# Performance work log

Measured on AMD Instinct MI355X. Metric: run time of the kernel, lower is better.

## Reference

```python
import jax, jax.numpy as jnp
import numpy as np
from jax import lax

B, L, V, E, H = 256, 512, 256, 256, 1024


def setup_inputs() -> dict:
    key = jax.random.key(0)
    k1, k2, k3, k4, k5 = jax.random.split(key, 5)
    x = jax.random.randint(k1, (B, L), 0, V, dtype=jnp.int64)
    hidden = jnp.zeros((B, H), dtype=jnp.float32)
    emb_table = jax.random.normal(k2, (V, E), dtype=jnp.float32)  # nn.Embedding default init ~N(0,1)
    W_e = 0.01 * jax.random.normal(k3, (E, H), dtype=jnp.float32)
    W_h = 0.01 * jax.random.normal(k4, (H, H), dtype=jnp.float32)
    W_o = 0.01 * jax.random.normal(k5, (H, V), dtype=jnp.float32)
    return {"x": x, "hidden": hidden, "emb_table": emb_table, "W_e": W_e, "W_h": W_h, "W_o": W_o}


def reference(x, hidden, emb_table, W_e, W_h, W_o):
    # Precompute input projection for all timesteps in one batched GEMM:
    # emb_table[x] : [B, L, E];  x_proj : [L, B, H] (time-major for scan)
    x_proj = jnp.einsum('ble,eh->lbh', emb_table[x], W_e)

    def step(h_prev, x_t):
        h_t = jnp.tanh(x_t + h_prev @ W_h)  # [B, H]
        return h_t, h_t

    final_hidden, outs = lax.scan(step, hidden, x_proj)  # outs: [L, B, H]
    # logits: [B, L, V]
    logits = jnp.einsum('lbh,hv->blv', outs, W_o)
    return logits, final_hidden
```

## Files before the change

### kernel.cpp

```cpp
#include <hip/hip_runtime.h>
#include <hip/hip_bf16.h>
#include <math.h>

#define B_ 256
#define L_ 512
#define V_ 256
#define E_ 256
#define H_ 1024
#define NSTEP_ 513

typedef float  f32x4  __attribute__((ext_vector_type(4)));
typedef short  bf16x8 __attribute__((ext_vector_type(8)));

static __device__ __forceinline__ ushort f2bf(float v) {
    __hip_bfloat16 b = __float2bfloat16(v);
    return *reinterpret_cast<ushort*>(&b);
}

__global__ void k_transpose_bf16(const float* __restrict__ in, ushort* __restrict__ out,
                                 int R, int C) {
    __shared__ float tile[64][65];
    int bx = blockIdx.x;
    int by = blockIdx.y;
    int tid = threadIdx.x;
    int g = tid >> 6, l = tid & 63;
    for (int i = 0; i < 16; ++i) {
        int r = g * 16 + i;
        tile[r][l] = in[(size_t)(by * 64 + r) * C + bx * 64 + l];
    }
    __syncthreads();
    for (int i = 0; i < 16; ++i) {
        int c = g * 16 + i;
        out[(size_t)(bx * 64 + c) * R + by * 64 + l] = f2bf(tile[l][c]);
    }
}

__global__ void k_f32_to_bf16(const float* __restrict__ in, ushort* __restrict__ out, int n) {
    int i = blockIdx.x * blockDim.x + threadIdx.x;
    if (i < n) out[i] = f2bf(in[i]);
}

__global__ void k_zero(unsigned* __restrict__ p, int n) {
    int i = blockIdx.x * blockDim.x + threadIdx.x;
    if (i < n) p[i] = 0u;
}

__global__ void k_proj(const float* __restrict__ emb, const float* __restrict__ We,
                       float* __restrict__ proj) {
    __shared__ float er[E_];
    int t = blockIdx.x;
    int h = blockIdx.y * 256 + threadIdx.x;
    er[threadIdx.x] = emb[t * E_ + threadIdx.x];
    __syncthreads();
    float acc = 0.f;
#pragma unroll 8
    for (int e = 0; e < E_; ++e) acc += er[e] * We[(size_t)e * H_ + h];
    proj[(size_t)t * H_ + h] = acc;
}

__global__ __launch_bounds__(256, 1) void k_scan(
    const int* __restrict__ x, const float* __restrict__ proj,
    const ushort* __restrict__ WhT, const ushort* __restrict__ WoT,
    ushort* __restrict__ ring, float* __restrict__ logits,
    float* __restrict__ final_h, unsigned* __restrict__ flags)
{
    __shared__ ushort lds_w[32 * 1024];
    __shared__ ushort lds_h[32 * 1024];
    __shared__ float  red[256 * 5];
    __shared__ ushort stile[32 * 32];

    int tid = threadIdx.x;
    int w = tid >> 6, lane = tid & 63;
    int l15 = lane & 15, l4 = lane >> 4;
    int bid = blockIdx.x;
    int rg = bid & 7;
    int cg = bid >> 3;
    int r0 = rg * 32, c0 = cg * 32;

    {
        const char* wsrc = (const char*)(WhT + (size_t)c0 * H_);
        char* wd = (char*)lds_w;
        for (int i = 0; i < 16; ++i) {
            int chunk = (w * 16 + i) * 1024;
            int o = chunk + lane * 16;
            int row = o >> 11, b = o & 2047;
            int so = row * 2048 + (b ^ ((row & 7) << 4));
            __builtin_amdgcn_global_load_lds(
                (const __attribute__((address_space(1))) void*)(wsrc + so),
                (__attribute__((address_space(3))) void*)(wd + chunk), 16, 0, 0);
        }
    }

    int a = w >> 1, bc = w & 1;
    int arow = a * 16 + l15;
    int brow = bc * 16 + l15;
    const char* ha = (const char*)lds_h + arow * 2048;
    const char* wa = (const char*)lds_w + brow * 2048;
    int as = (arow & 7) << 4, bs = (brow & 7) << 4;
    int gcol = c0 + bc * 16 + l15;

    int lrg = cg & 1, vcol0 = (cg >> 1) * 16;
    int srow = lrg * 16 + l15;
    const char* hbp = (const char*)lds_h + srow * 2048;
    int hs2 = (srow & 7) << 4;
    const ushort* wo = WoT + (size_t)(vcol0 + l15) * H_;
    int bbase = (w == 1) ? 0 : (w == 2) ? 11 : 22;
    int bcnt  = (w == 3) ? 10 : 11;

    for (int s = 0; s <= NSTEP_; ++s) {
        float pv[4];
        if (s < L_) {
#pragma unroll
            for (int j = 0; j < 4; ++j) {
                int grow = r0 + a * 16 + l4 * 4 + j;
                pv[j] = proj[(size_t)x[grow * L_ + s] * H_ + gcol];
            }
        }

        if (w == 0) {
            if (s >= 1 && s <= L_) {
                const unsigned* fp = flags + ((size_t)rg * NSTEP_ + s) * 32 + lane;
                unsigned v = 1u;
                while (true) {
                    if (lane < 32) {
                        asm volatile("global_load_dword %0, %1, off sc0 sc1\n\t"
                                     "s_waitcnt vmcnt(0)"
                                     : "=v"(v) : "v"(fp) : "memory");
                    }
                    if (__ballot(v != 0u) == ~0ull) break;
                }
            }
        } else if (s >= 2) {
            f32x4 lacc = {0.f, 0.f, 0.f, 0.f};
            for (int kk = 0; kk < bcnt; ++kk) {
                int k = (bbase + kk) * 32 + l4 * 8;
                bf16x8 af = *(const bf16x8*)(hbp + ((2 * k) ^ hs2));
                bf16x8 bf = *(const bf16x8*)(wo + k);
                lacc = __builtin_amdgcn_mfma_f32_16x16x32_bf16(af, bf, lacc, 0, 0, 0);
            }
#pragma unroll
            for (int j = 0; j < 4; ++j) red[tid * 5 + j] = lacc[j];
        }
        __syncthreads();

        f32x4 tv[16];
        if (s <= L_) {
            const char* hsrc = (const char*)(ring + (size_t)(s & 1) * B_ * H_
                                             + (size_t)r0 * H_) + tid * 16;
#pragma unroll
            for (int i = 0; i < 16; ++i) {
                asm volatile("global_load_dwordx4 %0, %1, off sc0 sc1"
                             : "=v"(tv[i]) : "v"(hsrc + i * 4096) : "memory");
            }
        }
        if (w == 0 && s >= 2) {
            int growb = r0 + lrg * 16 + l4 * 4;
#pragma unroll
            for (int j = 0; j < 4; ++j) {
                float ssum = red[(64 + lane) * 5 + j] + red[(128 + lane) * 5 + j]
                           + red[(192 + lane) * 5 + j];
                logits[((size_t)(growb + j) * L_ + (s - 2)) * V_ + vcol0 + l15] = ssum;
            }
        }
        if (s <= L_) {
            asm volatile("s_waitcnt vmcnt(0)" ::: "memory");
#pragma unroll
            for (int i = 0; i < 16; ++i) {
                int o = i * 4096 + tid * 16;
                int row = o >> 11, b = o & 2047;
                *(f32x4*)((char*)lds_h + row * 2048 + (b ^ ((row & 7) << 4))) = tv[i];
            }
        }
        __syncthreads();

        if (s < L_) {
            f32x4 acc0 = {0.f, 0.f, 0.f, 0.f};
            f32x4 acc1 = {0.f, 0.f, 0.f, 0.f};
#pragma unroll
            for (int kk = 0; kk < 32; kk += 2) {
                int kb0 = (kk * 32 + l4 * 8) * 2;
                int kb1 = ((kk + 1) * 32 + l4 * 8) * 2;
                bf16x8 af0 = *(const bf16x8*)(ha + (kb0 ^ as));
                bf16x8 bf0 = *(const bf16x8*)(wa + (kb0 ^ bs));
                bf16x8 af1 = *(const bf16x8*)(ha + (kb1 ^ as));
                bf16x8 bf1 = *(const bf16x8*)(wa + (kb1 ^ bs));
                acc0 = __builtin_amdgcn_mfma_f32_16x16x32_bf16(af0, bf0, acc0, 0, 0, 0);
                acc1 = __builtin_amdgcn_mfma_f32_16x16x32_bf16(af1, bf1, acc1, 0, 0, 0);
            }
#pragma unroll
            for (int j = 0; j < 4; ++j) {
                int lrow = a * 16 + l4 * 4 + j;
                float hv = tanhf((acc0[j] + acc1[j]) + pv[j]);
                stile[lrow * 32 + bc * 16 + l15] = f2bf(hv);
                if (s == L_ - 1) final_h[(size_t)(r0 + lrow) * H_ + gcol] = hv;
            }
            __syncthreads();
            if (tid < 128) {
                int row = tid >> 2, seg = tid & 3;
                f32x4 d = *(const f32x4*)&stile[row * 32 + seg * 8];
                char* dst = (char*)(ring + (size_t)((s + 1) & 1) * B_ * H_
                                    + (size_t)(r0 + row) * H_ + c0 + seg * 8);
                asm volatile("global_store_dwordx4 %0, %1, off sc0 sc1"
                             :: "v"(dst), "v"(d) : "memory");
            }
            asm volatile("s_waitcnt vmcnt(0)" ::: "memory");
            __syncthreads();
            if (tid == 0) {
                unsigned* fdst = flags + ((size_t)rg * NSTEP_ + (s + 1)) * 32 + cg;
                unsigned one = 1u;
                asm volatile("global_store_dword %0, %1, off sc0 sc1"
                             :: "v"(fdst), "v"(one) : "memory");
            }
        }
    }
}

extern "C" void kernel_launch(void* const* d_in, const int* in_sizes, int n_in,
                              void* d_out, int out_size, void* d_ws, size_t ws_size,
                              hipStream_t stream)
{
    const int*   x   = (const int*)d_in[0];
    const float* hid = (const float*)d_in[1];
    const float* emb = (const float*)d_in[2];
    const float* We  = (const float*)d_in[3];
    const float* Wh  = (const float*)d_in[4];
    const float* Wo  = (const float*)d_in[5];

    float* logits  = (float*)d_out;
    float* final_h = logits + (size_t)B_ * L_ * V_;

    char* ws = (char*)d_ws;
    float*    proj  = (float*)(ws);
    ushort*   WhT   = (ushort*)(ws + (1u << 20));
    ushort*   WoT   = (ushort*)(ws + 3u * (1u << 20));
    ushort*   ring  = (ushort*)(ws + 3u * (1u << 20) + (1u << 19));
    unsigned* flags = (unsigned*)(ws + 4u * (1u << 20) + (1u << 19));

    k_zero<<<dim3(NSTEP_), 256, 0, stream>>>(flags, 8 * NSTEP_ * 32);
    k_transpose_bf16<<<dim3(16, 16), 256, 0, stream>>>(Wh, WhT, H_, H_);
    k_transpose_bf16<<<dim3(4, 16),  256, 0, stream>>>(Wo, WoT, H_, V_);
    k_f32_to_bf16<<<dim3(1024), 256, 0, stream>>>(hid, ring, B_ * H_);
    k_proj<<<dim3(256, 4), 256, 0, stream>>>(emb, We, proj);

    k_scan<<<dim3(256), 256, 0, stream>>>(x, proj, WhT, WoT, ring,
                                          logits, final_h, flags);
}
```

Baseline: 2.433 ms.

## Split logits projection out of recurrent scan into chunked GEMM kernels over hidden-state ring

Before, each scan step also computed a slice of the output projection inside the persistent recurrence kernel. Now the scan kernel only runs the recurrence over chunks of timesteps and writes every hidden state into a multi-slot ring buffer. A separate k_logits kernel then computes the logits for each chunk as a larger batched GEMM. It also replaces tanhf with an exp-based tanh, shrinks the flags to bytes, and pads the staging tile. This shortens the serial critical path per step, but adds per-chunk kernel relaunches, reloads of the weight panel, and dependence on workspace size for the ring.

```diff
diff --git a/kernel.cpp b/kernel.cpp
--- a/kernel.cpp
+++ b/kernel.cpp
@@ -7,21 +7,26 @@
 #define V_ 256
 #define E_ 256
 #define H_ 1024
-#define NSTEP_ 513
 
 typedef float  f32x4  __attribute__((ext_vector_type(4)));
 typedef short  bf16x8 __attribute__((ext_vector_type(8)));
+typedef unsigned int u32;
+typedef unsigned char u8;
 
 static __device__ __forceinline__ ushort f2bf(float v) {
     __hip_bfloat16 b = __float2bfloat16(v);
     return *reinterpret_cast<ushort*>(&b);
 }
 
+static __device__ __forceinline__ float ftanh(float z) {
+    float e = __expf(2.f * z);
+    return 1.f - 2.f / (e + 1.f);
+}
+
 __global__ void k_transpose_bf16(const float* __restrict__ in, ushort* __restrict__ out,
                                  int R, int C) {
     __shared__ float tile[64][65];
-    int bx = blockIdx.x;
-    int by = blockIdx.y;
+    int bx = blockIdx.x, by = blockIdx.y;
     int tid = threadIdx.x;
     int g = tid >> 6, l = tid & 63;
     for (int i = 0; i < 16; ++i) {
@@ -40,7 +45,7 @@
     if (i < n) out[i] = f2bf(in[i]);
 }
 
-__global__ void k_zero(unsigned* __restrict__ p, int n) {
+__global__ void k_zero(u32* __restrict__ p, int n) {
     int i = blockIdx.x * blockDim.x + threadIdx.x;
     if (i < n) p[i] = 0u;
 }
@@ -59,22 +64,20 @@
 }
 
 __global__ __launch_bounds__(256, 1) void k_scan(
-    const int* __restrict__ x, const float* __restrict__ proj,
-    const ushort* __restrict__ WhT, const ushort* __restrict__ WoT,
-    ushort* __restrict__ ring, float* __restrict__ logits,
-    float* __restrict__ final_h, unsigned* __restrict__ flags)
+    const int* __restrict__ xs, const float* __restrict__ proj,
+    const ushort* __restrict__ WhT, ushort* __restrict__ ring,
+    float* __restrict__ final_h, u8* __restrict__ flags,
+    int t0, int Tc, int S)
 {
     __shared__ ushort lds_w[32 * 1024];
-    __shared__ ushort lds_h[32 * 1024];
-    __shared__ float  red[256 * 5];
-    __shared__ ushort stile[32 * 32];
+    __shared__ ushort panel[32 * 1024];
+    __shared__ ushort stile[32 * 40];
 
     int tid = threadIdx.x;
     int w = tid >> 6, lane = tid & 63;
     int l15 = lane & 15, l4 = lane >> 4;
     int bid = blockIdx.x;
-    int rg = bid & 7;
-    int cg = bid >> 3;
+    int rg = bid & 7, cg = bid >> 3;
     int r0 = rg * 32, c0 = cg * 32;
 
     {
@@ -92,127 +95,148 @@
     }
 
     int a = w >> 1, bc = w & 1;
-    int arow = a * 16 + l15;
-    int brow = bc * 16 + l15;
-    const char* ha = (const char*)lds_h + arow * 2048;
+    int arow = a * 16 + l15, brow = bc * 16 + l15;
+    const char* ha = (const char*)panel + arow * 2048;
     const char* wa = (const char*)lds_w + brow * 2048;
-    int as = (arow & 7) << 4, bs = (brow & 7) << 4;
+    int as_ = (arow & 7) << 4, bs = (brow & 7) << 4;
     int gcol = c0 + bc * 16 + l15;
 
-    int lrg = cg & 1, vcol0 = (cg >> 1) * 16;
-    int srow = lrg * 16 + l15;
-    const char* hbp = (const char*)lds_h + srow * 2048;
-    int hs2 = (srow & 7) << 4;
-    const ushort* wo = WoT + (size_t)(vcol0 + l15) * H_;
-    int bbase = (w == 1) ? 0 : (w == 2) ? 11 : 22;
-    int bcnt  = (w == 3) ? 10 : 11;
-
-    for (int s = 0; s <= NSTEP_; ++s) {
-        float pv[4];
-        if (s < L_) {
-#pragma unroll
-            for (int j = 0; j < 4; ++j) {
-                int grow = r0 + a * 16 + l4 * 4 + j;
-                pv[j] = proj[(size_t)x[grow * L_ + s] * H_ + gcol];
+    for (int s = 0; s < Tc; ++s) {
+        int t = t0 + s;
+        if (s > 0 && w == 0) {
+            const u8* fp = flags + (size_t)t * 256 + rg * 32 + lane;
+            u32 v = 1u;
+            while (true) {
+                if (lane < 32)
+                    asm volatile("global_load_ubyte %0, %1, off sc0 sc1\n\t"
+                                 "s_waitcnt vmcnt(0)" : "=v"(v) : "v"(fp) : "memory");
+                if (__ballot(v != 0u) == ~0ull) break;
             }
         }
-
-        if (w == 0) {
-            if (s >= 1 && s <= L_) {
-                const unsigned* fp = flags + ((size_t)rg * NSTEP_ + s) * 32 + lane;
-                unsigned v = 1u;
-                while (true) {
-                    if (lane < 32) {
-                        asm volatile("global_load_dword %0, %1, off sc0 sc1\n\t"
-                                     "s_waitcnt vmcnt(0)"
-                                     : "=v"(v) : "v"(fp) : "memory");
-                    }
-                    if (__ballot(v != 0u) == ~0ull) break;
-                }
-            }
-        } else if (s >= 2) {
-            f32x4 lacc = {0.f, 0.f, 0.f, 0.f};
-            for (int kk = 0; kk < bcnt; ++kk) {
-                int k = (bbase + kk) * 32 + l4 * 8;
-                bf16x8 af = *(const bf16x8*)(hbp + ((2 * k) ^ hs2));
-                bf16x8 bf = *(const bf16x8*)(wo + k);
-                lacc = __builtin_amdgcn_mfma_f32_16x16x32_bf16(af, bf, lacc, 0, 0, 0);
-            }
-#pragma unroll
-            for (int j = 0; j < 4; ++j) red[tid * 5 + j] = lacc[j];
-        }
-        __syncthreads();
-
-        f32x4 tv[16];
-        if (s <= L_) {
-            const char* hsrc = (const char*)(ring + (size_t)(s & 1) * B_ * H_
+        __syncthreads();
+
+        {
+            const char* hsrc = (const char*)(ring + (size_t)(t % S) * B_ * H_
                                              + (size_t)r0 * H_) + tid * 16;
-#pragma unroll
-            for (int i = 0; i < 16; ++i) {
-                asm volatile("global_load_dwordx4 %0, %1, off sc0 sc1"
+            f32x4 tv[16];
+#pragma unroll
+            for (int i = 0; i < 16; ++i)
+                asm volatile("global_load_dwordx4 %0, %1, off sc0"
                              : "=v"(tv[i]) : "v"(hsrc + i * 4096) : "memory");
-            }
-        }
-        if (w == 0 && s >= 2) {
-            int growb = r0 + lrg * 16 + l4 * 4;
-#pragma unroll
-            for (int j = 0; j < 4; ++j) {
-                float ssum = red[(64 + lane) * 5 + j] + red[(128 + lane) * 5 + j]
-                           + red[(192 + lane) * 5 + j];
-                logits[((size_t)(growb + j) * L_ + (s - 2)) * V_ + vcol0 + l15] = ssum;
-            }
-        }
-        if (s <= L_) {
             asm volatile("s_waitcnt vmcnt(0)" ::: "memory");
+            __builtin_amdgcn_sched_barrier(0);
 #pragma unroll
             for (int i = 0; i < 16; ++i) {
                 int o = i * 4096 + tid * 16;
                 int row = o >> 11, b = o & 2047;
-                *(f32x4*)((char*)lds_h + row * 2048 + (b ^ ((row & 7) << 4))) = tv[i];
+                *(f32x4*)((char*)panel + row * 2048 + (b ^ ((row & 7) << 4))) = tv[i];
             }
         }
         __syncthreads();
 
-        if (s < L_) {
-            f32x4 acc0 = {0.f, 0.f, 0.f, 0.f};
-            f32x4 acc1 = {0.f, 0.f, 0.f, 0.f};
-#pragma unroll
-            for (int kk = 0; kk < 32; kk += 2) {
-                int kb0 = (kk * 32 + l4 * 8) * 2;
-                int kb1 = ((kk + 1) * 32 + l4 * 8) * 2;
-                bf16x8 af0 = *(const bf16x8*)(ha + (kb0 ^ as));
-                bf16x8 bf0 = *(const bf16x8*)(wa + (kb0 ^ bs));
-                bf16x8 af1 = *(const bf16x8*)(ha + (kb1 ^ as));
-                bf16x8 bf1 = *(const bf16x8*)(wa + (kb1 ^ bs));
-                acc0 = __builtin_amdgcn_mfma_f32_16x16x32_bf16(af0, bf0, acc0, 0, 0, 0);
-                acc1 = __builtin_amdgcn_mfma_f32_16x16x32_bf16(af1, bf1, acc1, 0, 0, 0);
-            }
-#pragma unroll
-            for (int j = 0; j < 4; ++j) {
-                int lrow = a * 16 + l4 * 4 + j;
-                float hv = tanhf((acc0[j] + acc1[j]) + pv[j]);
-                stile[lrow * 32 + bc * 16 + l15] = f2bf(hv);
-                if (s == L_ - 1) final_h[(size_t)(r0 + lrow) * H_ + gcol] = hv;
-            }
-            __syncthreads();
-            if (tid < 128) {
-                int row = tid >> 2, seg = tid & 3;
-                f32x4 d = *(const f32x4*)&stile[row * 32 + seg * 8];
-                char* dst = (char*)(ring + (size_t)((s + 1) & 1) * B_ * H_
-                                    + (size_t)(r0 + row) * H_ + c0 + seg * 8);
-                asm volatile("global_store_dwordx4 %0, %1, off sc0 sc1"
-                             :: "v"(dst), "v"(d) : "memory");
-            }
-            asm volatile("s_waitcnt vmcnt(0)" ::: "memory");
-            __syncthreads();
-            if (tid == 0) {
-                unsigned* fdst = flags + ((size_t)rg * NSTEP_ + (s + 1)) * 32 + cg;
-                unsigned one = 1u;
-                asm volatile("global_store_dword %0, %1, off sc0 sc1"
-                             :: "v"(fdst), "v"(one) : "memory");
-            }
-        }
-    }
+        float pv[4];
+#pragma unroll
+        for (int j = 0; j < 4; ++j) {
+            int grow = r0 + a * 16 + l4 * 4 + j;
+            pv[j] = proj[(size_t)xs[grow * L_ + t] * H_ + gcol];
+        }
+        f32x4 acc0 = {0.f,0.f,0.f,0.f}, acc1 = {0.f,0.f,0.f,0.f};
+#pragma unroll
+        for (int kk = 0; kk < 32; kk += 2) {
+            int kb0 = (kk * 32 + l4 * 8) * 2;
+            int kb1 = ((kk + 1) * 32 + l4 * 8) * 2;
+            bf16x8 af0 = *(const bf16x8*)(ha + (kb0 ^ as_));
+            bf16x8 bf0 = *(const bf16x8*)(wa + (kb0 ^ bs));
+            bf16x8 af1 = *(const bf16x8*)(ha + (kb1 ^ as_));
+            bf16x8 bf1 = *(const bf16x8*)(wa + (kb1 ^ bs));
+            acc0 = __builtin_amdgcn_mfma_f32_16x16x32_bf16(af0, bf0, acc0, 0, 0, 0);
+            acc1 = __builtin_amdgcn_mfma_f32_16x16x32_bf16(af1, bf1, acc1, 0, 0, 0);
+        }
+#pragma unroll
+        for (int j = 0; j < 4; ++j) {
+            int lrow = a * 16 + l4 * 4 + j;
+            float hv = ftanh((acc0[j] + acc1[j]) + pv[j]);
+            stile[lrow * 40 + bc * 16 + l15] = f2bf(hv);
+            if (t == L_ - 1) final_h[(size_t)(r0 + lrow) * H_ + gcol] = hv;
+        }
+        __syncthreads();
+
+        if (tid < 128) {
+            int row = tid >> 2, seg = tid & 3;
+            f32x4 d = *(const f32x4*)&stile[row * 40 + seg * 8];
+            char* dst = (char*)(ring + (size_t)((t + 1) % S) * B_ * H_
+                                + (size_t)(r0 + row) * H_ + c0 + seg * 8);
+            asm volatile("global_store_dwordx4 %0, %1, off sc0 sc1"
+                         :: "v"(dst), "v"(d) : "memory");
+        }
+        asm volatile("s_waitcnt vmcnt(0)" ::: "memory");
+        __syncthreads();
+        if (tid == 0) {
+            u8* fdst = flags + (size_t)(t + 1) * 256 + rg * 32 + cg;
+            u32 one = 1u;
+            asm volatile("global_store_byte %0, %1, off sc0 sc1"
+                         :: "v"(fdst), "v"(one) : "memory");
+        }
+    }
+}
+
+__global__ __launch_bounds__(256, 1) void k_logits(
+    const ushort* __restrict__ ring, const ushort* __restrict__ WoT,
+    float* __restrict__ logits, int t0, int S)
+{
+    __shared__ ushort Ap[64 * 1024];
+    int tid = threadIdx.x;
+    int w = tid >> 6, lane = tid & 63;
+    int l15 = lane & 15, l4 = lane >> 4;
+    int bid = blockIdx.x;
+    int tl = bid >> 2, q = bid & 3;
+    int t = t0 + tl, slot = (t + 1) % S;
+
+    {
+        const char* asrc = (const char*)(ring + (size_t)slot * B_ * H_
+                                         + (size_t)(q * 64) * H_);
+        char* ad = (char*)Ap;
+        for (int i = 0; i < 32; ++i) {
+            int chunk = (w * 32 + i) * 1024;
+            int o = chunk + lane * 16;
+            int row = o >> 11, b = o & 2047;
+            int so = row * 2048 + (b ^ ((row & 7) << 4));
+            __builtin_amdgcn_global_load_lds(
+                (const __attribute__((address_space(1))) void*)(asrc + so),
+                (__attribute__((address_space(3))) void*)(ad + chunk), 16, 0, 0);
+        }
+    }
+    asm volatile("s_waitcnt vmcnt(0)" ::: "memory");
+    __syncthreads();
+
+    int arow = w * 16 + l15;
+    const char* ha = (const char*)Ap + (size_t)arow * 2048;
+    int as_ = (arow & 7) << 4;
+    bf16x8 af[32];
+#pragma unroll
+    for (int kk = 0; kk < 32; ++kk) {
+        int kb = (kk * 32 + l4 * 8) * 2;
+        af[kk] = *(const bf16x8*)(ha + (kb ^ as_));
+    }
+    f32x4 acc[16];
+#pragma unroll
+    for (int vs = 0; vs < 16; ++vs) acc[vs] = (f32x4){0.f, 0.f, 0.f, 0.f};
+    const ushort* wob = WoT + (size_t)l15 * H_ + l4 * 8;
+#pragma unroll
+    for (int kk = 0; kk < 32; ++kk) {
+#pragma unroll
+        for (int vs = 0; vs < 16; ++vs) {
+            bf16x8 bfr = *(const bf16x8*)(wob + (size_t)(vs * 16) * H_ + kk * 32);
+            acc[vs] = __builtin_amdgcn_mfma_f32_16x16x32_bf16(af[kk], bfr, acc[vs], 0, 0, 0);
+        }
+    }
+#pragma unroll
+    for (int vs = 0; vs < 16; ++vs)
+#pragma unroll
+        for (int j = 0; j < 4; ++j) {
+            int brow = q * 64 + w * 16 + l4 * 4 + j;
+            logits[(size_t)brow * (L_ * V_) + (size_t)t * V_ + vs * 16 + l15] = acc[vs][j];
+        }
 }
 
 extern "C" void kernel_launch(void* const* d_in, const int* in_sizes, int n_in,
@@ -230,18 +254,29 @@
     float* final_h = logits + (size_t)B_ * L_ * V_;
 
     char* ws = (char*)d_ws;
-    float*    proj  = (float*)(ws);
-    ushort*   WhT   = (ushort*)(ws + (1u << 20));
-    ushort*   WoT   = (ushort*)(ws + 3u * (1u << 20));
-    ushort*   ring  = (ushort*)(ws + 3u * (1u << 20) + (1u << 19));
-    unsigned* flags = (unsigned*)(ws + 4u * (1u << 20) + (1u << 19));
-
-    k_zero<<<dim3(NSTEP_), 256, 0, stream>>>(flags, 8 * NSTEP_ * 32);
+    float*  proj  = (float*)(ws);
+    ushort* WhT   = (ushort*)(ws + (1u << 20));
+    ushort* WoT   = (ushort*)(ws + 3u * (1u << 20));
+    u8*     flags = (u8*)(ws + 3u * (1u << 20) + (1u << 19));
+    const size_t RING_OFF = 3u * (1u << 20) + (1u << 19) + (1u << 18);
+    ushort* ring  = (ushort*)(ws + RING_OFF);
+    const size_t SLOT = (size_t)B_ * H_ * 2u;
+
+    int S = (int)(ws_size > RING_OFF ? (ws_size - RING_OFF) / SLOT : 0);
+    if (S > 65) S = 65;
+    if (S < 2)  S = 2;
+
+    k_zero<<<dim3(129), 256, 0, stream>>>((u32*)flags, 513 * 256 / 4);
     k_transpose_bf16<<<dim3(16, 16), 256, 0, stream>>>(Wh, WhT, H_, H_);
     k_transpose_bf16<<<dim3(4, 16),  256, 0, stream>>>(Wo, WoT, H_, V_);
     k_f32_to_bf16<<<dim3(1024), 256, 0, stream>>>(hid, ring, B_ * H_);
     k_proj<<<dim3(256, 4), 256, 0, stream>>>(emb, We, proj);
 
-    k_scan<<<dim3(256), 256, 0, stream>>>(x, proj, WhT, WoT, ring,
-                                          logits, final_h, flags);
-}
+    int T = S - 1;
+    for (int t0 = 0; t0 < L_; t0 += T) {
+        int Tc = (L_ - t0 < T) ? (L_ - t0) : T;
+        k_scan<<<dim3(256), 256, 0, stream>>>(x, proj, WhT, ring,
+                                              final_h, flags, t0, Tc, S);
+        k_logits<<<dim3(4 * Tc), 256, 0, stream>>>(ring, WoT, logits, t0, S);
+    }
+}
```

New measurement: 3.119 ms. +28.2%, slower.
